# Optimization experiments

Measured on AMD Instinct MI355X. Metric: run time of the kernel, lower is better.

## Reference

```python
import jax, jax.numpy as jnp
import numpy as np

N = 50000        # nodes
E = 600000       # edges (before self-loops)
IN_DIM = 128
HID = 128
EMB = 128
DEC = 64
B = 1024         # drug pairs
NEG_GAT = 0.2    # GATConv leaky-relu slope
NEG_DEC = 0.1    # decoder LeakyReLU slope
EPS = 1e-5       # BatchNorm eps


def setup_inputs() -> dict:
    key = jax.random.key(0)
    ks = jax.random.split(key, 16)
    rn = lambda k, s, sc=0.05: jax.random.normal(k, s, dtype=jnp.float32) * sc
    return dict(
        x=rn(ks[0], (N, IN_DIM), 1.0),
        edge_index=jax.random.randint(ks[1], (2, E), 0, N, dtype=jnp.int32),
        drug_index=jax.random.randint(ks[2], (B, 2), 1, N + 1, dtype=jnp.int32),
        W1=rn(ks[3], (HID, IN_DIM)), att1=rn(ks[4], (1, 1, 2 * HID)), b1=jnp.zeros((HID,), jnp.float32),
        g1=jnp.ones((HID,), jnp.float32), be1=jnp.zeros((HID,), jnp.float32),
        W2=rn(ks[5], (HID, HID)), att2=rn(ks[6], (1, 1, 2 * HID)), b2=jnp.zeros((HID,), jnp.float32),
        g2=jnp.ones((HID,), jnp.float32), be2=jnp.zeros((HID,), jnp.float32),
        W3=rn(ks[7], (EMB, HID)), att3=rn(ks[8], (1, 1, 2 * EMB)), b3=jnp.zeros((EMB,), jnp.float32),
        g3=jnp.ones((EMB,), jnp.float32), be3=jnp.zeros((EMB,), jnp.float32),
        P1=rn(ks[9], (EMB, DEC), 0.1), P2=rn(ks[10], (DEC, DEC), 0.1),
    )


def _segment_softmax(alpha, seg, n):
    amax = jax.ops.segment_max(alpha, seg, num_segments=n)
    amax = jnp.where(jnp.isfinite(amax), amax, 0.0)
    ex = jnp.exp(alpha - amax[seg])
    den = jax.ops.segment_sum(ex, seg, num_segments=n)
    return ex / (den[seg] + 1e-16)


def _gat(x, src, dst, W, att, b):
    # num_head == 1 (required by original att-parameter shape)
    n = x.shape[0]
    d = W.shape[0]
    h = (x @ W.T)[:, None, :]                    # [N,1,d]
    x_i, x_j = h[dst], h[src]                    # target, source per edge
    # alpha = (cat([x_i,x_j],-1)*att).sum(-1) without materializing the concat
    alpha = (x_i * att[..., :d]).sum(-1) + (x_j * att[..., d:]).sum(-1)  # [E,1]
    alpha = jax.nn.leaky_relu(alpha, NEG_GAT)
    # NOTE: original code softmaxes over edge_index[0] (src) while aggregating by dst
    alpha = _segment_softmax(alpha, src, n)
    out = jax.ops.segment_sum(x_j * alpha[:, :, None], dst, num_segments=n)
    return jax.nn.relu(out.reshape(n, -1) + b)


def _bn(x, g, b):
    # BatchNorm1d (training-mode batch statistics, biased var)
    mu = x.mean(0)
    var = x.var(0)
    return (x - mu) * jax.lax.rsqrt(var + EPS) * g + b


def reference(x, edge_index, drug_index, W1, att1, b1, g1, be1,
              W2, att2, b2, g2, be2, W3, att3, b3, g3, be3, P1, P2):
    n = x.shape[0]
    loops = jnp.arange(n, dtype=edge_index.dtype)
    src = jnp.concatenate([edge_index[0], loops])  # add_self_loops
    dst = jnp.concatenate([edge_index[1], loops])
    h = jax.nn.leaky_relu(_bn(_gat(x, src, dst, W1, att1, b1), g1, be1), NEG_DEC)
    h = jax.nn.leaky_relu(_bn(_gat(h, src, dst, W2, att2, b2), g2, be2), NEG_DEC)
    h = jax.nn.leaky_relu(_bn(_gat(h, src, dst, W3, att3, b3), g3, be3), NEG_DEC)
    a = h[drug_index[:, 0] - 1]                    # [B,EMB]
    bvec = h[drug_index[:, 1] - 1]                 # [B,EMB]
    M = P1 @ P2 @ P1.T                             # [EMB,EMB] bilinear form
    ypred = jnp.einsum('bd,de,be->b', a, M, bvec)[:, None]  # [B,1]
    return ypred
```

## Files before the change

kernel.cpp:

```cpp
#include <hip/hip_runtime.h>
#include <hip/hip_bf16.h>

#define DEVINL __device__ __forceinline__

constexpr int N  = 50000;
constexpr int E  = 600000;
constexpr int TE = E + N;
constexpr int D  = 128;
constexpr int GEMM_ROWS = 64;
constexpr int GEMM_B = (N + GEMM_ROWS - 1) / GEMM_ROWS;
constexpr int HST_STRIDE = 136;

constexpr int NBUCK = (N + 255) >> 8;
constexpr int NSB   = 2 * NBUCK;
constexpr int CHUNK = 2560;
constexpr int EB3   = (TE + CHUNK - 1) / CHUNK;
constexpr int EB3P  = 256;

typedef short bf16x8 __attribute__((ext_vector_type(8)));
typedef float f32x4  __attribute__((ext_vector_type(4)));

DEVINL float lrelu(float x, float s) { return x >= 0.f ? x : s * x; }

DEVINL unsigned short f2bf(float f) {
    unsigned u = __float_as_uint(f);
    u += 0x7FFFu + ((u >> 16) & 1u);
    return (unsigned short)(u >> 16);
}
DEVINL float bfl(unsigned u) { return __uint_as_float(u << 16); }
DEVINL float bfh(unsigned u) { return __uint_as_float(u & 0xFFFF0000u); }

__global__ __launch_bounds__(256) void k_wb3(const float* __restrict__ W0,
                                             const float* __restrict__ W1,
                                             const float* __restrict__ W2,
                                             unsigned short* __restrict__ Wb) {
    int b = blockIdx.x;
    int l = b >> 6;
    const float* W = (l == 0) ? W0 : (l == 1) ? W1 : W2;
    int t = (b & 63) * 256 + threadIdx.x;
    Wb[l * 16384 + t] = f2bf(W[t]);
}

__global__ __launch_bounds__(256) void k_gemm(const float* __restrict__ X,
                                              const unsigned short* __restrict__ O16,
                                              const unsigned short* __restrict__ Wb,
                                              unsigned short* __restrict__ Hb16,
                                              const float* __restrict__ att,
                                              float* __restrict__ ai,
                                              float* __restrict__ ajx,
                                              const float* __restrict__ csum,
                                              const float* __restrict__ csq,
                                              const float* __restrict__ g,
                                              const float* __restrict__ be,
                                              int apply_bn) {
    __shared__ unsigned short hst[4][16][HST_STRIDE];
    __shared__ float ssl[256];
    int wave = threadIdx.x >> 6, lane = threadIdx.x & 63;
    int m = lane & 15, quad = lane >> 4;
    int r0 = blockIdx.x * GEMM_ROWS + wave * 16;

    if (apply_bn) {
        if (threadIdx.x < 128) {
            int c = threadIdx.x;
            float mean = csum[c] / (float)N;
            float var  = csq[c] / (float)N - mean * mean;
            float scale = g[c] * rsqrtf(var + 1e-5f);
            ssl[c] = scale;
            ssl[128 + c] = be[c] - mean * scale;
        }
        __syncthreads();
    }

    bf16x8 afrag[4];
    int rowA = r0 + m;
    bool rowok = rowA < N;
    #pragma unroll
    for (int k4 = 0; k4 < 4; k4++) {
        int c0 = k4 * 32 + quad * 8;
        float v[8];
        if (rowok) {
            if (apply_bn) {
                uint4 hu = *(const uint4*)(O16 + (size_t)rowA * D + c0);
                v[0] = bfl(hu.x); v[1] = bfh(hu.x);
                v[2] = bfl(hu.y); v[3] = bfh(hu.y);
                v[4] = bfl(hu.z); v[5] = bfh(hu.z);
                v[6] = bfl(hu.w); v[7] = bfh(hu.w);
                #pragma unroll
                for (int j = 0; j < 8; j++)
                    v[j] = lrelu(v[j] * ssl[c0 + j] + ssl[128 + c0 + j], 0.1f);
            } else {
                float4 x0 = *(const float4*)(X + (size_t)rowA * D + c0);
                float4 x1 = *(const float4*)(X + (size_t)rowA * D + c0 + 4);
                v[0] = x0.x; v[1] = x0.y; v[2] = x0.z; v[3] = x0.w;
                v[4] = x1.x; v[5] = x1.y; v[6] = x1.z; v[7] = x1.w;
            }
        } else {
            #pragma unroll
            for (int j = 0; j < 8; j++) v[j] = 0.f;
        }
        #pragma unroll
        for (int j = 0; j < 8; j++) afrag[k4][j] = (short)f2bf(v[j]);
    }

    float pii[4] = {0.f, 0.f, 0.f, 0.f};
    float pjj[4] = {0.f, 0.f, 0.f, 0.f};
    #pragma unroll
    for (int nt = 0; nt < 8; nt++) {
        int n0 = nt * 16;
        f32x4 acc = {0.f, 0.f, 0.f, 0.f};
        const unsigned short* wrow = Wb + (size_t)(n0 + m) * D + quad * 8;
        #pragma unroll
        for (int k4 = 0; k4 < 4; k4++) {
            bf16x8 b = *(const bf16x8*)(wrow + k4 * 32);
            acc = __builtin_amdgcn_mfma_f32_16x16x32_bf16(afrag[k4], b, acc, 0, 0, 0);
        }
        float ad = att[n0 + m];
        float as = att[128 + n0 + m];
        #pragma unroll
        for (int i = 0; i < 4; i++) {
            hst[wave][quad * 4 + i][n0 + m] = f2bf(acc[i]);
            pii[i] += acc[i] * ad;
            pjj[i] += acc[i] * as;
        }
    }

    #pragma unroll
    for (int t = 0; t < 4; t++) {
        int r = t * 4 + quad;
        int row = r0 + r;
        int cb = m * 8;
        uint4 vv = *(const uint4*)&hst[wave][r][cb];
        if (row < N)
            *(uint4*)(Hb16 + (size_t)row * D + cb) = vv;
    }

    #pragma unroll
    for (int mask = 8; mask >= 1; mask >>= 1) {
        #pragma unroll
        for (int i = 0; i < 4; i++) {
            pii[i] += __shfl_xor(pii[i], mask);
            pjj[i] += __shfl_xor(pjj[i], mask);
        }
    }
    if (m == 0) {
        #pragma unroll
        for (int i = 0; i < 4; i++) {
            int row = r0 + quad * 4 + i;
            if (row < N) { ai[row] = pii[i]; ajx[2 * (size_t)row] = pjj[i]; }
        }
    }
}

DEVINL void edge_sd(int e, const int* ei, int& s, int& d) {
    if (e < E) { s = ei[e]; d = ei[E + e]; }
    else       { s = d = e - E; }
}

__global__ __launch_bounds__(256) void k_cnt(const int* __restrict__ ei,
                                             unsigned* __restrict__ hist) {
    __shared__ unsigned cnt[NSB];
    for (int t = threadIdx.x; t < NSB; t += 256) cnt[t] = 0;
    __syncthreads();
    int base = blockIdx.x * CHUNK;
    for (int i = threadIdx.x; i < CHUNK; i += 256) {
        int e = base + i;
        if (e < TE) {
            int s, d; edge_sd(e, ei, s, d);
            atomicAdd(&cnt[d >> 8], 1u);
            atomicAdd(&cnt[NBUCK + (s >> 8)], 1u);
        }
    }
    __syncthreads();
    unsigned* row = hist + (size_t)blockIdx.x * NSB;
    for (int t = threadIdx.x; t < NSB; t += 256) row[t] = cnt[t];
}

__global__ __launch_bounds__(256) void k_bscan(const unsigned* __restrict__ hist,
                                               unsigned* __restrict__ pref,
                                               unsigned* __restrict__ btot) {
    __shared__ unsigned sc[256];
    int sb = blockIdx.x, t = threadIdx.x;
    unsigned v = (t < EB3) ? hist[(size_t)t * NSB + sb] : 0;
    sc[t] = v;
    __syncthreads();
    #pragma unroll
    for (int off = 1; off < 256; off <<= 1) {
        unsigned add = (t >= off) ? sc[t - off] : 0;
        __syncthreads();
        sc[t] += add;
        __syncthreads();
    }
    if (t < EB3) pref[(size_t)sb * EB3P + t] = sc[t] - v;
    if (t == EB3 - 1) btot[sb] = sc[t];
}

__global__ __launch_bounds__(256) void k_boff(const unsigned* __restrict__ btot,
                                              unsigned* __restrict__ boff2,
                                              int* __restrict__ ptrbase) {
    __shared__ unsigned sc[256];
    int t = threadIdx.x;
    for (int side = 0; side < 2; side++) {
        unsigned v = (t < NBUCK) ? btot[side * NBUCK + t] : 0;
        sc[t] = v;
        __syncthreads();
        #pragma unroll
        for (int off = 1; off < 256; off <<= 1) {
            unsigned add = (t >= off) ? sc[t - off] : 0;
            __syncthreads();
            sc[t] += add;
            __syncthreads();
        }
        if (t < NBUCK) boff2[side * (NBUCK + 1) + t] = sc[t] - v;
        if (t == NBUCK - 1) boff2[side * (NBUCK + 1) + NBUCK] = sc[t];
        __syncthreads();
    }
    if (t == 0) { ptrbase[N] = TE; ptrbase[(N + 8) + N] = TE; }
}

__global__ __launch_bounds__(256) void k_scatter(const int* __restrict__ ei,
                                                 const unsigned* __restrict__ pref,
                                                 const unsigned* __restrict__ boff2,
                                                 unsigned* __restrict__ sorted) {
    __shared__ unsigned alloc[NSB];
    int j = blockIdx.x;
    for (int t = threadIdx.x; t < NSB; t += 256) {
        int side = t >= NBUCK;
        int bucket = t - side * NBUCK;
        alloc[t] = boff2[side * (NBUCK + 1) + bucket] + pref[(size_t)t * EB3P + j]
                 + (side ? (unsigned)TE : 0u);
    }
    __syncthreads();
    int base = j * CHUNK;
    for (int i = threadIdx.x; i < CHUNK; i += 256) {
        int e = base + i;
        if (e < TE) {
            int s, d; edge_sd(e, ei, s, d);
            unsigned pd = atomicAdd(&alloc[d >> 8], 1u);
            sorted[pd] = ((unsigned)(d & 255) << 16) | (unsigned)s;
            unsigned ps = atomicAdd(&alloc[NBUCK + (s >> 8)], 1u);
            sorted[ps] = ((unsigned)(s & 255) << 16) | (unsigned)d;
        }
    }
}

__global__ __launch_bounds__(256) void k_csr(const unsigned* __restrict__ sorted,
                                             const unsigned* __restrict__ boff2,
                                             int* __restrict__ ptrbase,
                                             unsigned short* __restrict__ srcc,
                                             unsigned short* __restrict__ dstc) {
    __shared__ unsigned cnt[256];
    __shared__ unsigned sc[256];
    int sb = blockIdx.x, t = threadIdx.x;
    int side = sb >= NBUCK;
    int bucket = sb - side * NBUCK;
    unsigned beg = boff2[side * (NBUCK + 1) + bucket];
    unsigned end = boff2[side * (NBUCK + 1) + bucket + 1];
    const unsigned* srt = sorted + (side ? (size_t)TE : 0);
    unsigned short* out = side ? dstc : srcc;
    int* ptr = ptrbase + (size_t)side * (N + 8);
    cnt[t] = 0;
    __syncthreads();
    for (unsigned idx = beg + t; idx < end; idx += 256)
        atomicAdd(&cnt[srt[idx] >> 16], 1u);
    __syncthreads();
    unsigned own = cnt[t];
    sc[t] = own;
    __syncthreads();
    #pragma unroll
    for (int off = 1; off < 256; off <<= 1) {
        unsigned add = (t >= off) ? sc[t - off] : 0;
        __syncthreads();
        sc[t] += add;
        __syncthreads();
    }
    unsigned loc = sc[t] - own;
    int v = (bucket << 8) + t;
    if (v < N) ptr[v] = (int)(beg + loc);
    cnt[t] = beg + loc;
    __syncthreads();
    for (unsigned idx = beg + t; idx < end; idx += 256) {
        unsigned u = srt[idx];
        unsigned pos = atomicAdd(&cnt[u >> 16], 1u);
        out[pos] = (unsigned short)u;
    }
}

__global__ __launch_bounds__(256) void k_den(const int* __restrict__ srcp,
                                             const unsigned short* __restrict__ dstc,
                                             const float* __restrict__ ai,
                                             float* __restrict__ ajx,
                                             float* __restrict__ csumz) {
    if (blockIdx.x == 0) csumz[threadIdx.x] = 0.f;
    int g = threadIdx.x >> 4, l16 = threadIdx.x & 15;
    int v = blockIdx.x * 16 + g;
    if (v >= N) return;
    int beg = srcp[v], end = srcp[v + 1];
    float ajv = ajx[2 * (size_t)v];
    float acc = 0.f;
    for (int idx = beg + l16; idx < end; idx += 16) {
        int d = dstc[idx];
        acc += expf(lrelu(ai[d] + ajv, 0.2f));
    }
    #pragma unroll
    for (int mask = 8; mask >= 1; mask >>= 1) acc += __shfl_xor(acc, mask);
    if (l16 == 0) ajx[2 * (size_t)v + 1] = 1.0f / (acc + 1e-16f);
}

__global__ __launch_bounds__(256) void k_aggregate(const int* __restrict__ rowp,
                                                   const unsigned short* __restrict__ srcc,
                                                   const float* __restrict__ ai,
                                                   const float2* __restrict__ ajinv,
                                                   const uint2* __restrict__ Hu2,
                                                   const float* __restrict__ bvec,
                                                   unsigned short* __restrict__ O16) {
    int wid = threadIdx.x >> 6, lane = threadIdx.x & 63;
    int h = lane >> 5, l32 = lane & 31;
    int v = blockIdx.x * 4 + wid;
    if (v >= N) return;
    int beg = rowp[v], end = rowp[v + 1];
    float aiv = ai[v];
    float a0 = 0.f, a1 = 0.f, a2 = 0.f, a3 = 0.f;
    int idx = beg;
    for (; idx + 8 <= end; idx += 8) {
        int    s[4];
        float2 aw[4];
        uint2  u[4];
        #pragma unroll
        for (int t = 0; t < 4; t++) s[t] = srcc[idx + 2 * t + h];
        #pragma unroll
        for (int t = 0; t < 4; t++) aw[t] = ajinv[s[t]];
        #pragma unroll
        for (int t = 0; t < 4; t++) u[t] = Hu2[(size_t)s[t] * 32 + l32];
        #pragma unroll
        for (int t = 0; t < 4; t++) {
            float w = expf(lrelu(aiv + aw[t].x, 0.2f)) * aw[t].y;
            a0 += w * bfl(u[t].x);
            a1 += w * bfh(u[t].x);
            a2 += w * bfl(u[t].y);
            a3 += w * bfh(u[t].y);
        }
    }
    for (; idx + 2 <= end; idx += 2) {
        int s = srcc[idx + h];
        float2 aw = ajinv[s];
        float w = expf(lrelu(aiv + aw.x, 0.2f)) * aw.y;
        uint2 u = Hu2[(size_t)s * 32 + l32];
        a0 += w * bfl(u.x);
        a1 += w * bfh(u.x);
        a2 += w * bfl(u.y);
        a3 += w * bfh(u.y);
    }
    if (idx < end) {
        int s = srcc[idx];
        float2 aw = ajinv[s];
        float w = (h == 0) ? expf(lrelu(aiv + aw.x, 0.2f)) * aw.y : 0.f;
        uint2 u = Hu2[(size_t)s * 32 + l32];
        a0 += w * bfl(u.x);
        a1 += w * bfh(u.x);
        a2 += w * bfl(u.y);
        a3 += w * bfh(u.y);
    }
    a0 += __shfl_xor(a0, 32);
    a1 += __shfl_xor(a1, 32);
    a2 += __shfl_xor(a2, 32);
    a3 += __shfl_xor(a3, 32);
    if (h == 0) {
        float4 b = ((const float4*)bvec)[l32];
        float o0 = fmaxf(a0 + b.x, 0.f);
        float o1 = fmaxf(a1 + b.y, 0.f);
        float o2 = fmaxf(a2 + b.z, 0.f);
        float o3 = fmaxf(a3 + b.w, 0.f);
        uint2 st;
        st.x = (unsigned)f2bf(o0) | ((unsigned)f2bf(o1) << 16);
        st.y = (unsigned)f2bf(o2) | ((unsigned)f2bf(o3) << 16);
        *(uint2*)(O16 + (size_t)v * D + l32 * 4) = st;
    }
}

__global__ __launch_bounds__(256) void k_stats(const unsigned short* __restrict__ O16,
                                               float* __restrict__ colsum, float* __restrict__ colsq) {
    int c4 = (threadIdx.x & 31) * 4;
    int rg = threadIdx.x >> 5;
    float s0=0.f,s1=0.f,s2=0.f,s3=0.f,q0=0.f,q1=0.f,q2=0.f,q3=0.f;
    for (int v = blockIdx.x * 8 + rg; v < N; v += gridDim.x * 8) {
        uint2 u = *(const uint2*)(O16 + (size_t)v * D + c4);
        float v0 = bfl(u.x), v1 = bfh(u.x), v2 = bfl(u.y), v3 = bfh(u.y);
        s0 += v0; q0 += v0 * v0;
        s1 += v1; q1 += v1 * v1;
        s2 += v2; q2 += v2 * v2;
        s3 += v3; q3 += v3 * v3;
    }
    __shared__ float ls[8][128], lq[8][128];
    ls[rg][c4+0]=s0; ls[rg][c4+1]=s1; ls[rg][c4+2]=s2; ls[rg][c4+3]=s3;
    lq[rg][c4+0]=q0; lq[rg][c4+1]=q1; lq[rg][c4+2]=q2; lq[rg][c4+3]=q3;
    __syncthreads();
    if (threadIdx.x < 128) {
        int c = threadIdx.x;
        float s = 0.f, q = 0.f;
        #pragma unroll
        for (int r = 0; r < 8; r++) { s += ls[r][c]; q += lq[r][c]; }
        atomicAdd(colsum + c, s);
        atomicAdd(colsq + c, q);
    }
}

__global__ __launch_bounds__(256) void k_T(const float* __restrict__ P1, const float* __restrict__ P2,
                                           float* __restrict__ T) {
    int t = blockIdx.x * 256 + threadIdx.x;
    if (t >= 128 * 64) return;
    int i = t >> 6, d = t & 63;
    float s = 0.f;
    #pragma unroll 8
    for (int k = 0; k < 64; k++) s += P1[i * 64 + k] * P2[k * 64 + d];
    T[t] = s;
}

__global__ __launch_bounds__(256) void k_M(const float* __restrict__ T, const float* __restrict__ P1,
                                           float* __restrict__ M) {
    int t = blockIdx.x * 256 + threadIdx.x;
    if (t >= 128 * 128) return;
    int i = t >> 7, j = t & 127;
    float s = 0.f;
    #pragma unroll 8
    for (int d = 0; d < 64; d++) s += T[i * 64 + d] * P1[j * 64 + d];
    M[t] = s;
}

__global__ __launch_bounds__(128) void k_pred(const unsigned short* __restrict__ O16,
                                              const float* __restrict__ csum,
                                              const float* __restrict__ csq,
                                              const float* __restrict__ g,
                                              const float* __restrict__ be,
                                              const int* __restrict__ drug,
                                              const float* __restrict__ M,
                                              float* __restrict__ out) {
    int b = blockIdx.x, i = threadIdx.x;
    __shared__ float av[128], bv[128];
    int ia = drug[b * 2] - 1, ib = drug[b * 2 + 1] - 1;
    float mean = csum[i] / (float)N;
    float var  = csq[i] / (float)N - mean * mean;
    float scale = g[i] * rsqrtf(var + 1e-5f);
    float shift = be[i] - mean * scale;
    float ha = __uint_as_float(((unsigned)O16[(size_t)ia * D + i]) << 16);
    float hb = __uint_as_float(((unsigned)O16[(size_t)ib * D + i]) << 16);
    av[i] = lrelu(ha * scale + shift, 0.1f);
    bv[i] = lrelu(hb * scale + shift, 0.1f);
    __syncthreads();
    const float4* M4  = (const float4*)(M + (size_t)i * 128);
    const float4* bv4 = (const float4*)bv;
    float u = 0.f;
    #pragma unroll 8
    for (int j = 0; j < 32; j++) {
        float4 mv = M4[j];
        float4 bb = bv4[j];
        u += mv.x * bb.x + mv.y * bb.y + mv.z * bb.z + mv.w * bb.w;
    }
    float val = av[i] * u;
    #pragma unroll
    for (int off = 32; off; off >>= 1) val += __shfl_down(val, off);
    __shared__ float red[2];
    if ((i & 63) == 0) red[i >> 6] = val;
    __syncthreads();
    if (i == 0) out[b] = red[0] + red[1];
}

extern "C" void kernel_launch(void* const* d_in, const int* in_sizes, int n_in,
                              void* d_out, int out_size, void* d_ws, size_t ws_size,
                              hipStream_t stream) {
    const float* x    = (const float*)d_in[0];
    const int*   ei   = (const int*)  d_in[1];
    const int*   drug = (const int*)  d_in[2];
    const float* W[3]   = {(const float*)d_in[3], (const float*)d_in[8],  (const float*)d_in[13]};
    const float* att[3] = {(const float*)d_in[4], (const float*)d_in[9],  (const float*)d_in[14]};
    const float* bb[3]  = {(const float*)d_in[5], (const float*)d_in[10], (const float*)d_in[15]};
    const float* gg[3]  = {(const float*)d_in[6], (const float*)d_in[11], (const float*)d_in[16]};
    const float* be[3]  = {(const float*)d_in[7], (const float*)d_in[12], (const float*)d_in[17]};
    const float* P1 = (const float*)d_in[18];
    const float* P2 = (const float*)d_in[19];

    float* ws = (float*)d_ws;
    size_t o_H      = 0;
    size_t o_O      = o_H + (size_t)N * 64;
    size_t o_ai     = o_O + (size_t)N * 64;
    size_t o_ajinv  = o_ai + N;
    size_t o_colsum = o_ajinv + 2 * (size_t)N;
    size_t o_colsq  = o_colsum + 128;
    size_t o_hist   = o_colsq + 128;
    size_t o_pref   = o_hist + (size_t)EB3 * NSB;
    size_t o_btot   = o_pref + (size_t)NSB * EB3P;
    size_t o_boff2  = o_btot + 512;
    size_t o_sorted = o_boff2 + 512;
    size_t o_rowptr = o_sorted + 2 * (size_t)TE;
    size_t o_srcp   = o_rowptr + N + 8;
    size_t o_src    = o_srcp + N + 8;
    size_t o_dstc   = o_src + TE / 2 + 8;
    size_t o_T      = o_dstc + TE / 2 + 8;
    size_t o_Mm     = o_T + 128 * 64;
    size_t o_Wb     = o_Mm + 128 * 128;

    unsigned short* Hb16 = (unsigned short*)(ws + o_H);
    uint2*          Hu2  = (uint2*)(ws + o_H);
    unsigned short* O16  = (unsigned short*)(ws + o_O);
    float*    ai    = ws + o_ai;
    float*    ajx   = ws + o_ajinv;
    float2*   ajinv = (float2*)(ws + o_ajinv);
    float*    csum  = ws + o_colsum;
    float*    csq   = ws + o_colsq;
    unsigned* hist  = (unsigned*)(ws + o_hist);
    unsigned* pref  = (unsigned*)(ws + o_pref);
    unsigned* btot  = (unsigned*)(ws + o_btot);
    unsigned* boff2 = (unsigned*)(ws + o_boff2);
    unsigned* sorted= (unsigned*)(ws + o_sorted);
    int*      rowp  = (int*)(ws + o_rowptr);
    int*      srcp  = (int*)(ws + o_srcp);
    unsigned short* srcc = (unsigned short*)(ws + o_src);
    unsigned short* dstc = (unsigned short*)(ws + o_dstc);
    float*    Tm    = ws + o_T;
    float*    Mm    = ws + o_Mm;
    unsigned short* Wb = (unsigned short*)(ws + o_Wb);

    const int NB4  = (N + 3) / 4;
    const int NB16 = (N + 15) / 16;

    k_cnt    <<<EB3, 256, 0, stream>>>(ei, hist);
    k_bscan  <<<NSB, 256, 0, stream>>>(hist, pref, btot);
    k_boff   <<<1,   256, 0, stream>>>(btot, boff2, rowp);
    k_scatter<<<EB3, 256, 0, stream>>>(ei, pref, boff2, sorted);
    k_csr    <<<NSB, 256, 0, stream>>>(sorted, boff2, rowp, srcc, dstc);

    k_wb3<<<192, 256, 0, stream>>>(W[0], W[1], W[2], Wb);

    for (int l = 0; l < 3; l++) {
        k_gemm<<<GEMM_B, 256, 0, stream>>>(x, O16, Wb + l * 16384, Hb16, att[l],
                                           ai, ajx, csum, csq, gg[l == 0 ? 0 : l - 1],
                                           be[l == 0 ? 0 : l - 1], l > 0 ? 1 : 0);
        k_den<<<NB16, 256, 0, stream>>>(srcp, dstc, ai, ajx, csum);
        k_aggregate<<<NB4, 256, 0, stream>>>(rowp, srcc, ai, ajinv, Hu2, bb[l], O16);
        k_stats<<<256, 256, 0, stream>>>(O16, csum, csq);
    }

    k_T<<<32, 256, 0, stream>>>(P1, P2, Tm);
    k_M<<<64, 256, 0, stream>>>(Tm, P1, Mm);
    k_pred<<<1024, 128, 0, stream>>>(O16, csum, csq, gg[2], be[2], drug, Mm, (float*)d_out);
}
```

Before: 389.1 us.

## Fuse setup kernels into one launch and process two row tiles per wave in GEMM

```diff
diff --git a/kernel.cpp b/kernel.cpp
--- a/kernel.cpp
+++ b/kernel.cpp
@@ -7,7 +7,7 @@
 constexpr int E  = 600000;
 constexpr int TE = E + N;
 constexpr int D  = 128;
-constexpr int GEMM_ROWS = 64;
+constexpr int GEMM_ROWS = 128;
 constexpr int GEMM_B = (N + GEMM_ROWS - 1) / GEMM_ROWS;
 constexpr int HST_STRIDE = 136;
 
@@ -17,6 +17,10 @@
 constexpr int EB3   = (TE + CHUNK - 1) / CHUNK;
 constexpr int EB3P  = 256;
 
+constexpr int FUSE_CNT = EB3;
+constexpr int FUSE_WB  = FUSE_CNT + 192;
+constexpr int FUSE_TM  = FUSE_WB + 64;
+
 typedef short bf16x8 __attribute__((ext_vector_type(8)));
 typedef float f32x4  __attribute__((ext_vector_type(4)));
 
@@ -30,15 +34,62 @@
 DEVINL float bfl(unsigned u) { return __uint_as_float(u << 16); }
 DEVINL float bfh(unsigned u) { return __uint_as_float(u & 0xFFFF0000u); }
 
-__global__ __launch_bounds__(256) void k_wb3(const float* __restrict__ W0,
-                                             const float* __restrict__ W1,
-                                             const float* __restrict__ W2,
-                                             unsigned short* __restrict__ Wb) {
+DEVINL void edge_sd(int e, const int* ei, int& s, int& d) {
+    if (e < E) { s = ei[e]; d = ei[E + e]; }
+    else       { s = d = e - E; }
+}
+
+__global__ __launch_bounds__(256) void k_fused0(const int* __restrict__ ei,
+                                                unsigned* __restrict__ hist,
+                                                const float* __restrict__ W0,
+                                                const float* __restrict__ W1,
+                                                const float* __restrict__ W2,
+                                                unsigned short* __restrict__ Wb,
+                                                const float* __restrict__ P1,
+                                                const float* __restrict__ P2,
+                                                float* __restrict__ Mm) {
+    __shared__ float smem[8192];
     int b = blockIdx.x;
-    int l = b >> 6;
-    const float* W = (l == 0) ? W0 : (l == 1) ? W1 : W2;
-    int t = (b & 63) * 256 + threadIdx.x;
-    Wb[l * 16384 + t] = f2bf(W[t]);
+    if (b < FUSE_CNT) {
+        unsigned* cnt = (unsigned*)smem;
+        for (int t = threadIdx.x; t < NSB; t += 256) cnt[t] = 0;
+        __syncthreads();
+        int base = b * CHUNK;
+        for (int i = threadIdx.x; i < CHUNK; i += 256) {
+            int e = base + i;
+            if (e < TE) {
+                int s, d; edge_sd(e, ei, s, d);
+                atomicAdd(&cnt[d >> 8], 1u);
+                atomicAdd(&cnt[NBUCK + (s >> 8)], 1u);
+            }
+        }
+        __syncthreads();
+        unsigned* row = hist + (size_t)b * NSB;
+        for (int t = threadIdx.x; t < NSB; t += 256) row[t] = cnt[t];
+    } else if (b < FUSE_WB) {
+        int bb = b - FUSE_CNT;
+        int l = bb >> 6;
+        const float* W = (l == 0) ? W0 : (l == 1) ? W1 : W2;
+        int t = (bb & 63) * 256 + threadIdx.x;
+        Wb[l * 16384 + t] = f2bf(W[t]);
+    } else {
+        int bb = b - FUSE_WB;
+        for (int idx = threadIdx.x; idx < 8192; idx += 256) {
+            int i = idx >> 6, d = idx & 63;
+            float s = 0.f;
+            #pragma unroll 8
+            for (int k = 0; k < 64; k++) s += P1[i * 64 + k] * P2[k * 64 + d];
+            smem[idx] = s;
+        }
+        __syncthreads();
+        int t = bb * 256 + threadIdx.x;
+        int i = t >> 7, j = t & 127;
+        const float* Trow = smem + i * 64;
+        float s = 0.f;
+        #pragma unroll 8
+        for (int d = 0; d < 64; d++) s += Trow[d] * P1[j * 64 + d];
+        Mm[t] = s;
+    }
 }
 
 __global__ __launch_bounds__(256) void k_gemm(const float* __restrict__ X,
@@ -53,11 +104,11 @@
                                               const float* __restrict__ g,
                                               const float* __restrict__ be,
                                               int apply_bn) {
-    __shared__ unsigned short hst[4][16][HST_STRIDE];
+    __shared__ unsigned short hst[4][32][HST_STRIDE];
     __shared__ float ssl[256];
     int wave = threadIdx.x >> 6, lane = threadIdx.x & 63;
     int m = lane & 15, quad = lane >> 4;
-    int r0 = blockIdx.x * GEMM_ROWS + wave * 16;
+    int r0 = blockIdx.x * GEMM_ROWS + wave * 32;
 
     if (apply_bn) {
         if (threadIdx.x < 128) {
@@ -71,61 +122,69 @@
         __syncthreads();
     }
 
-    bf16x8 afrag[4];
-    int rowA = r0 + m;
-    bool rowok = rowA < N;
-    #pragma unroll
-    for (int k4 = 0; k4 < 4; k4++) {
-        int c0 = k4 * 32 + quad * 8;
-        float v[8];
-        if (rowok) {
-            if (apply_bn) {
-                uint4 hu = *(const uint4*)(O16 + (size_t)rowA * D + c0);
-                v[0] = bfl(hu.x); v[1] = bfh(hu.x);
-                v[2] = bfl(hu.y); v[3] = bfh(hu.y);
-                v[4] = bfl(hu.z); v[5] = bfh(hu.z);
-                v[6] = bfl(hu.w); v[7] = bfh(hu.w);
+    bf16x8 afrag[2][4];
+    #pragma unroll
+    for (int tile = 0; tile < 2; tile++) {
+        int rowA = r0 + tile * 16 + m;
+        bool rowok = rowA < N;
+        #pragma unroll
+        for (int k4 = 0; k4 < 4; k4++) {
+            int c0 = k4 * 32 + quad * 8;
+            float v[8];
+            if (rowok) {
+                if (apply_bn) {
+                    uint4 hu = *(const uint4*)(O16 + (size_t)rowA * D + c0);
+                    v[0] = bfl(hu.x); v[1] = bfh(hu.x);
+                    v[2] = bfl(hu.y); v[3] = bfh(hu.y);
+                    v[4] = bfl(hu.z); v[5] = bfh(hu.z);
+                    v[6] = bfl(hu.w); v[7] = bfh(hu.w);
+                    #pragma unroll
+                    for (int j = 0; j < 8; j++)
+                        v[j] = lrelu(v[j] * ssl[c0 + j] + ssl[128 + c0 + j], 0.1f);
+                } else {
+                    float4 x0 = *(const float4*)(X + (size_t)rowA * D + c0);
+                    float4 x1 = *(const float4*)(X + (size_t)rowA * D + c0 + 4);
+                    v[0] = x0.x; v[1] = x0.y; v[2] = x0.z; v[3] = x0.w;
+                    v[4] = x1.x; v[5] = x1.y; v[6] = x1.z; v[7] = x1.w;
+                }
+            } else {
                 #pragma unroll
-                for (int j = 0; j < 8; j++)
-                    v[j] = lrelu(v[j] * ssl[c0 + j] + ssl[128 + c0 + j], 0.1f);
-            } else {
-                float4 x0 = *(const float4*)(X + (size_t)rowA * D + c0);
-                float4 x1 = *(const float4*)(X + (size_t)rowA * D + c0 + 4);
-                v[0] = x0.x; v[1] = x0.y; v[2] = x0.z; v[3] = x0.w;
-                v[4] = x1.x; v[5] = x1.y; v[6] = x1.z; v[7] = x1.w;
+                for (int j = 0; j < 8; j++) v[j] = 0.f;
             }
-        } else {
             #pragma unroll
-            for (int j = 0; j < 8; j++) v[j] = 0.f;
-        }
-        #pragma unroll
-        for (int j = 0; j < 8; j++) afrag[k4][j] = (short)f2bf(v[j]);
-    }
-
-    float pii[4] = {0.f, 0.f, 0.f, 0.f};
-    float pjj[4] = {0.f, 0.f, 0.f, 0.f};
+            for (int j = 0; j < 8; j++) afrag[tile][k4][j] = (short)f2bf(v[j]);
+        }
+    }
+
+    float pii[2][4] = {{0.f,0.f,0.f,0.f},{0.f,0.f,0.f,0.f}};
+    float pjj[2][4] = {{0.f,0.f,0.f,0.f},{0.f,0.f,0.f,0.f}};
     #pragma unroll
     for (int nt = 0; nt < 8; nt++) {
         int n0 = nt * 16;
-        f32x4 acc = {0.f, 0.f, 0.f, 0.f};
+        f32x4 acc0 = {0.f, 0.f, 0.f, 0.f};
+        f32x4 acc1 = {0.f, 0.f, 0.f, 0.f};
         const unsigned short* wrow = Wb + (size_t)(n0 + m) * D + quad * 8;
         #pragma unroll
         for (int k4 = 0; k4 < 4; k4++) {
-            bf16x8 b = *(const bf16x8*)(wrow + k4 * 32);
-            acc = __builtin_amdgcn_mfma_f32_16x16x32_bf16(afrag[k4], b, acc, 0, 0, 0);
+            bf16x8 bfr = *(const bf16x8*)(wrow + k4 * 32);
+            acc0 = __builtin_amdgcn_mfma_f32_16x16x32_bf16(afrag[0][k4], bfr, acc0, 0, 0, 0);
+            acc1 = __builtin_amdgcn_mfma_f32_16x16x32_bf16(afrag[1][k4], bfr, acc1, 0, 0, 0);
         }
         float ad = att[n0 + m];
         float as = att[128 + n0 + m];
         #pragma unroll
         for (int i = 0; i < 4; i++) {
-            hst[wave][quad * 4 + i][n0 + m] = f2bf(acc[i]);
-            pii[i] += acc[i] * ad;
-            pjj[i] += acc[i] * as;
-        }
-    }
-
-    #pragma unroll
-    for (int t = 0; t < 4; t++) {
+            hst[wave][quad * 4 + i][n0 + m]      = f2bf(acc0[i]);
+            hst[wave][16 + quad * 4 + i][n0 + m] = f2bf(acc1[i]);
+            pii[0][i] += acc0[i] * ad;
+            pjj[0][i] += acc0[i] * as;
+            pii[1][i] += acc1[i] * ad;
+            pjj[1][i] += acc1[i] * as;
+        }
+    }
+
+    #pragma unroll
+    for (int t = 0; t < 8; t++) {
         int r = t * 4 + quad;
         int row = r0 + r;
         int cb = m * 8;
@@ -137,42 +196,24 @@
     #pragma unroll
     for (int mask = 8; mask >= 1; mask >>= 1) {
         #pragma unroll
-        for (int i = 0; i < 4; i++) {
-            pii[i] += __shfl_xor(pii[i], mask);
-            pjj[i] += __shfl_xor(pjj[i], mask);
+        for (int tile = 0; tile < 2; tile++) {
+            #pragma unroll
+            for (int i = 0; i < 4; i++) {
+                pii[tile][i] += __shfl_xor(pii[tile][i], mask);
+                pjj[tile][i] += __shfl_xor(pjj[tile][i], mask);
+            }
         }
     }
     if (m == 0) {
         #pragma unroll
-        for (int i = 0; i < 4; i++) {
-            int row = r0 + quad * 4 + i;
-            if (row < N) { ai[row] = pii[i]; ajx[2 * (size_t)row] = pjj[i]; }
-        }
-    }
-}
-
-DEVINL void edge_sd(int e, const int* ei, int& s, int& d) {
-    if (e < E) { s = ei[e]; d = ei[E + e]; }
-    else       { s = d = e - E; }
-}
-
-__global__ __launch_bounds__(256) void k_cnt(const int* __restrict__ ei,
-                                             unsigned* __restrict__ hist) {
-    __shared__ unsigned cnt[NSB];
-    for (int t = threadIdx.x; t < NSB; t += 256) cnt[t] = 0;
-    __syncthreads();
-    int base = blockIdx.x * CHUNK;
-    for (int i = threadIdx.x; i < CHUNK; i += 256) {
-        int e = base + i;
-        if (e < TE) {
-            int s, d; edge_sd(e, ei, s, d);
-            atomicAdd(&cnt[d >> 8], 1u);
-            atomicAdd(&cnt[NBUCK + (s >> 8)], 1u);
-        }
-    }
-    __syncthreads();
-    unsigned* row = hist + (size_t)blockIdx.x * NSB;
-    for (int t = threadIdx.x; t < NSB; t += 256) row[t] = cnt[t];
+        for (int tile = 0; tile < 2; tile++) {
+            #pragma unroll
+            for (int i = 0; i < 4; i++) {
+                int row = r0 + tile * 16 + quad * 4 + i;
+                if (row < N) { ai[row] = pii[tile][i]; ajx[2 * (size_t)row] = pjj[tile][i]; }
+            }
+        }
+    }
 }
 
 __global__ __launch_bounds__(256) void k_bscan(const unsigned* __restrict__ hist,
@@ -404,28 +445,6 @@
     }
 }
 
-__global__ __launch_bounds__(256) void k_T(const float* __restrict__ P1, const float* __restrict__ P2,
-                                           float* __restrict__ T) {
-    int t = blockIdx.x * 256 + threadIdx.x;
-    if (t >= 128 * 64) return;
-    int i = t >> 6, d = t & 63;
-    float s = 0.f;
-    #pragma unroll 8
-    for (int k = 0; k < 64; k++) s += P1[i * 64 + k] * P2[k * 64 + d];
-    T[t] = s;
-}
-
-__global__ __launch_bounds__(256) void k_M(const float* __restrict__ T, const float* __restrict__ P1,
-                                           float* __restrict__ M) {
-    int t = blockIdx.x * 256 + threadIdx.x;
-    if (t >= 128 * 128) return;
-    int i = t >> 7, j = t & 127;
-    float s = 0.f;
-    #pragma unroll 8
-    for (int d = 0; d < 64; d++) s += T[i * 64 + d] * P1[j * 64 + d];
-    M[t] = s;
-}
-
 __global__ __launch_bounds__(128) void k_pred(const unsigned short* __restrict__ O16,
                                               const float* __restrict__ csum,
                                               const float* __restrict__ csq,
@@ -494,8 +513,7 @@
     size_t o_srcp   = o_rowptr + N + 8;
     size_t o_src    = o_srcp + N + 8;
     size_t o_dstc   = o_src + TE / 2 + 8;
-    size_t o_T      = o_dstc + TE / 2 + 8;
-    size_t o_Mm     = o_T + 128 * 64;
+    size_t o_Mm     = o_dstc + TE / 2 + 8;
     size_t o_Wb     = o_Mm + 128 * 128;
 
     unsigned short* Hb16 = (unsigned short*)(ws + o_H);
@@ -515,20 +533,18 @@
     int*      srcp  = (int*)(ws + o_srcp);
     unsigned short* srcc = (unsigned short*)(ws + o_src);
     unsigned short* dstc = (unsigned short*)(ws + o_dstc);
-    float*    Tm    = ws + o_T;
     float*    Mm    = ws + o_Mm;
     unsigned short* Wb = (unsigned short*)(ws + o_Wb);
 
     const int NB4  = (N + 3) / 4;
     const int NB16 = (N + 15) / 16;
 
-    k_cnt    <<<EB3, 256, 0, stream>>>(ei, hist);
+    k_fused0<<<FUSE_TM, 256, 0, stream>>>(ei, hist, W[0], W[1], W[2], Wb, P1, P2, Mm);
+
     k_bscan  <<<NSB, 256, 0, stream>>>(hist, pref, btot);
     k_boff   <<<1,   256, 0, stream>>>(btot, boff2, rowp);
     k_scatter<<<EB3, 256, 0, stream>>>(ei, pref, boff2, sorted);
     k_csr    <<<NSB, 256, 0, stream>>>(sorted, boff2, rowp, srcc, dstc);
-
-    k_wb3<<<192, 256, 0, stream>>>(W[0], W[1], W[2], Wb);
 
     for (int l = 0; l < 3; l++) {
         k_gemm<<<GEMM_B, 256, 0, stream>>>(x, O16, Wb + l * 16384, Hb16, att[l],
@@ -539,7 +555,5 @@
         k_stats<<<256, 256, 0, stream>>>(O16, csum, csq);
     }
 
-    k_T<<<32, 256, 0, stream>>>(P1, P2, Tm);
-    k_M<<<64, 256, 0, stream>>>(Tm, P1, Mm);
     k_pred<<<1024, 128, 0, stream>>>(O16, csum, csq, gg[2], be[2], drug, Mm, (float*)d_out);
 }
```

Result: slower. 402.5 us (+3.4%).
